# Performance work log

Hardware: AMD Instinct MI355X
Metric: run time of the kernel (lower is better)

The kernel has to match this reference:

```python
import jax, jax.numpy as jnp
import numpy as np

DIM = 128        # per-head dim == model width in this module
Q_HEADS = 16
KV_HEADS = 4
WINDOW = 512
BATCH = 4
SEQ = 2048


def setup_inputs() -> dict:
    key = jax.random.key(0)
    k1, k2, k3 = jax.random.split(key, 3)
    x = jax.random.normal(k1, (BATCH, SEQ, DIM), dtype=jnp.float32)
    # fused qkv weight, stored (in, out) so forward is x @ W_qkv
    W_qkv = jax.random.normal(k2, (DIM, (Q_HEADS + 2 * KV_HEADS) * DIM), dtype=jnp.float32) * (DIM ** -0.5)
    W_proj = jax.random.normal(k3, (Q_HEADS * DIM, DIM), dtype=jnp.float32) * ((Q_HEADS * DIM) ** -0.5)
    return {"x": x, "W_qkv": W_qkv, "W_proj": W_proj}


def _gqa_forward(x, W_qkv, W_proj):
    b, s, d = x.shape
    qkv = x @ W_qkv                                    # [b, s, (Hq+2Hkv)*d]
    qkv = qkv.reshape(b, s, Q_HEADS + 2 * KV_HEADS, d).transpose(0, 2, 1, 3)
    q = qkv[:, :Q_HEADS]                               # [b, Hq, s, d]
    k = qkv[:, Q_HEADS:Q_HEADS + KV_HEADS]             # [b, Hkv, s, d]
    v = qkv[:, Q_HEADS + KV_HEADS:]                    # [b, Hkv, s, d]

    # GQA: repeat kv heads to match q heads
    group = Q_HEADS // KV_HEADS
    k = jnp.repeat(k, group, axis=1)                   # [b, Hq, s, d]
    v = jnp.repeat(v, group, axis=1)

    scale = 1.0 / jnp.sqrt(jnp.float32(d))
    scores = jnp.einsum('bhqd,bhkd->bhqk', q, k) * scale   # [b, Hq, s, s]

    q_idx = jnp.arange(s)[:, None]
    kv_idx = jnp.arange(s)[None, :]
    rel = (q_idx - kv_idx).astype(jnp.float32)         # [s, s]
    # per-head ALiBi slope: exp2(-(h+1)*8/Hq), added (sign matches source)
    h = jnp.arange(Q_HEADS, dtype=jnp.float32)
    slopes = jnp.exp2(-((h + 1.0) * 8.0 / Q_HEADS))    # [Hq]
    scores = scores + slopes[None, :, None, None] * rel[None, None, :, :]

    mask = (q_idx >= kv_idx) & ((q_idx - kv_idx) <= WINDOW)
    scores = jnp.where(mask[None, None], scores, -jnp.inf)
    probs = jax.nn.softmax(scores, axis=-1)

    att = jnp.einsum('bhqk,bhkd->bhqd', probs, v)      # [b, Hq, s, d]
    att = att.transpose(0, 2, 1, 3).reshape(b, s, Q_HEADS * d)
    return att @ W_proj                                # [b, s, d]


def reference(x, W_qkv, W_proj):
    return _gqa_forward(x, W_qkv, W_proj)
```

## Files before the change

### kernel.cpp

```cpp
#include <hip/hip_runtime.h>
#include <math.h>

#define DIM_    128
#define QH_     16
#define KVH_    4
#define WIN_    512
#define BATCH_  4
#define SEQ_    2048
#define QKV_LD  3072

#define QB_LD   3136
#define VG_LD   2112
#define AH_LD   2112
#define WP_LD   2112

#define NX   (BATCH_*SEQ_*DIM_)
#define NWQ  (DIM_*QKV_LD)

typedef __attribute__((ext_vector_type(8))) short short8;
typedef __attribute__((ext_vector_type(4))) float f32x4;
typedef unsigned short u16;
typedef unsigned int u32;

__device__ __forceinline__ u16 f2bf(float f) {
    u32 u = __float_as_uint(f);
    u += 0x7fff + ((u >> 16) & 1);
    return (u16)(u >> 16);
}
__device__ __forceinline__ float bf2f(u16 u) {
    return __uint_as_float(((u32)u) << 16);
}
__device__ __forceinline__ u32 pkbf(float a, float b) {
    u32 r;
    __asm__("v_cvt_pk_bf16_f32 %0, %1, %2" : "=v"(r) : "v"(a), "v"(b));
    return r;
}
#define MFMA16 __builtin_amdgcn_mfma_f32_16x16x32_bf16

#if __has_builtin(__builtin_amdgcn_exp2f)
#define EXP2F __builtin_amdgcn_exp2f
#else
#define EXP2F exp2f
#endif

__device__ __forceinline__ void gload_lds16(const u16* g, u16* l) {
    __builtin_amdgcn_global_load_lds(
        (const __attribute__((address_space(1))) unsigned int*)(const void*)g,
        (__attribute__((address_space(3))) unsigned int*)(void*)l, 16, 0, 0);
}

__global__ __launch_bounds__(256) void prep(
    const float* __restrict__ x, const float* __restrict__ Wqkv,
    const float* __restrict__ Wproj,
    u16* __restrict__ xh, u16* __restrict__ wth, u16* __restrict__ wpth)
{
    if (blockIdx.x < 1024) {
        const size_t t = (size_t)blockIdx.x * 256 + threadIdx.x;
        float4 v = *(const float4*)(x + 4 * t);
        ushort4 o;
        o.x = f2bf(v.x); o.y = f2bf(v.y); o.z = f2bf(v.z); o.w = f2bf(v.w);
        *(ushort4*)(xh + 4 * t) = o;
        return;
    }
    __shared__ float T[32][33];
    int tile = blockIdx.x - 1024;
    const float* src; u16* dst; int N, ldo;
    if (tile < 384) { src = Wqkv;  dst = wth;  N = 3072; ldo = 128; }
    else { tile -= 384; src = Wproj; dst = wpth; N = 128; ldo = WP_LD; }
    const int ntile = N >> 5;
    const int k0 = (tile / ntile) << 5, n0 = (tile % ntile) << 5;
    const int tx = threadIdx.x & 31, ty = threadIdx.x >> 5;
    #pragma unroll
    for (int i = 0; i < 4; ++i)
        T[ty + 8 * i][tx] = src[(size_t)(k0 + ty + 8 * i) * N + n0 + tx];
    __syncthreads();
    #pragma unroll
    for (int i = 0; i < 4; ++i)
        dst[(size_t)(n0 + ty + 8 * i) * ldo + k0 + tx] = f2bf(T[tx][ty + 8 * i]);
}

__global__ __launch_bounds__(256) void gemm1_mfma(
    const u16* __restrict__ xh, const u16* __restrict__ wth,
    u16* __restrict__ qkvb, u16* __restrict__ vg)
{
    const int bn = blockIdx.x * 256;
    const int mc = blockIdx.y * 128;
    const int tid = threadIdx.x;
    const int wv = tid >> 6, lane = tid & 63;
    const int lo = lane & 15, hi = lane >> 4;
    const int lr = lo, quad = hi;
    const int wn = bn + wv * 64;

    __shared__ u16 Ct[2][16][264];

    short8 bf[4][4];
    #pragma unroll
    for (int nt = 0; nt < 4; ++nt)
        #pragma unroll
        for (int s = 0; s < 4; ++s)
            bf[nt][s] = *(const short8*)(
                wth + (size_t)(wn + nt * 16 + lo) * DIM_ + s * 32 + hi * 8);

    const bool qk = (bn < 2560);
    const u16* aA = xh + (size_t)(mc + lo) * DIM_ + hi * 8;
    const int sr = tid >> 4, sc = tid & 15;

#define G1BODY(AF, IT) do {                                                   \
    f32x4 acc[4] = {};                                                        \
    if (qk) {                                                                 \
        _Pragma("unroll")                                                     \
        for (int s = 0; s < 4; ++s)                                           \
            _Pragma("unroll")                                                 \
            for (int nt = 0; nt < 4; ++nt)                                    \
                acc[nt] = MFMA16(bf[nt][s], AF[s], acc[nt], 0, 0, 0);         \
        const int bufq = (IT) & 1;                                            \
        _Pragma("unroll")                                                     \
        for (int nt = 0; nt < 4; ++nt) {                                      \
            uint2 o;                                                          \
            o.x = pkbf(acc[nt][0], acc[nt][1]);                               \
            o.y = pkbf(acc[nt][2], acc[nt][3]);                               \
            *(uint2*)&Ct[bufq][lr][wv * 64 + nt * 16 + quad * 4] = o;         \
        }                                                                     \
        __syncthreads();                                                      \
        const int row = mc + (IT) * 16 + sr;                                  \
        u16* drow = qkvb + (size_t)row * QB_LD + bn;                          \
        short8 v0 = *(const short8*)&Ct[bufq][sr][sc * 8];                    \
        short8 v1 = *(const short8*)&Ct[bufq][sr][128 + sc * 8];              \
        *(short8*)(drow + sc * 8) = v0;                                       \
        *(short8*)(drow + 128 + sc * 8) = v1;                                 \
    } else {                                                                  \
        _Pragma("unroll")                                                     \
        for (int s = 0; s < 4; ++s)                                           \
            _Pragma("unroll")                                                 \
            for (int nt = 0; nt < 4; ++nt)                                    \
                acc[nt] = MFMA16(AF[s], bf[nt][s], acc[nt], 0, 0, 0);         \
        const int m0 = mc + (IT) * 16 + quad * 4;                             \
        const int bb = m0 >> 11, mseq = m0 & 2047;                            \
        _Pragma("unroll")                                                     \
        for (int nt = 0; nt < 4; ++nt) {                                      \
            const int ncol = wn + nt * 16 + lr - 2560;                        \
            const int kvh = ncol >> 7, d = ncol & 127;                        \
            uint2 o;                                                          \
            o.x = pkbf(acc[nt][0], acc[nt][1]);                               \
            o.y = pkbf(acc[nt][2], acc[nt][3]);                               \
            *(uint2*)(vg + ((size_t)(bb * KVH_ + kvh) * DIM_ + d) * VG_LD     \
                      + mseq) = o;                                            \
        }                                                                     \
    }                                                                         \
} while (0)

    short8 afA[4], afB[4];
    #pragma unroll
    for (int s = 0; s < 4; ++s) afA[s] = *(const short8*)(aA + s * 32);

    #pragma unroll 1
    for (int it = 0; it < 8; it += 2) {
        const u16* aN = aA + (size_t)(it + 1) * 16 * DIM_;
        #pragma unroll
        for (int s = 0; s < 4; ++s) afB[s] = *(const short8*)(aN + s * 32);
        G1BODY(afA, it);
        const int nx = (it + 2 < 8) ? (it + 2) : 7;
        const u16* aN2 = aA + (size_t)nx * 16 * DIM_;
        #pragma unroll
        for (int s = 0; s < 4; ++s) afA[s] = *(const short8*)(aN2 + s * 32);
        G1BODY(afB, it + 1);
    }
#undef G1BODY
}

__global__ __launch_bounds__(512) void attn_mfma(
    const u16* __restrict__ qkvb, const u16* __restrict__ vg,
    u16* __restrict__ ah)
{
    const int xcd  = blockIdx.x & 7;
    const int idx  = blockIdx.x >> 3;
    const int pair = xcd + 8 * (idx & 1);
    const int qt   = idx >> 1;
    const int b    = pair >> 2, kvh = pair & 3;
    const int q0 = qt << 5;
    const int tid = threadIdx.x;
    const int wv8 = tid >> 6, lane = tid & 63;
    const int hq = wv8 >> 1, mrow = wv8 & 1;
    const int lr = lane & 15, quad = lane >> 4;
    const int h = kvh * 4 + hq;
    const bool oddq = (quad & 1) != 0;

    __shared__ u16 Kb[3][8][512];
    __shared__ u16 Vb[3][8][512];

    const float scale2 = 0.08838834764831845f * 1.4426950408889634f;
    const float slope2 = exp2f(-0.5f * (float)(h + 1)) * 1.4426950408889634f;
    const int jbase = max(0, q0 - WIN_);
    const int nch = (q0 + 32 - jbase) >> 5;
    const size_t rowb = (size_t)b * SEQ_;
    const u16* kg  = qkvb + rowb * QB_LD + (QH_ + kvh) * DIM_;
    const u16* vgb = vg + (size_t)(b * KVH_ + kvh) * DIM_ * VG_LD;
    const int lo = lane & 15, hi = lane >> 4;

    short8 qf[4];
    {
        const u16* qp = qkvb + (rowb + q0 + mrow * 16 + lr) * QB_LD
                        + h * DIM_ + quad * 8;
        #pragma unroll
        for (int s = 0; s < 4; ++s) qf[s] = *(const short8*)(qp + 32 * s);
    }

    float alpha0;
    {
        const int q = q0 + mrow * 16 + lr;
        const int rm = (q < WIN_) ? q : WIN_;
        alpha0 = slope2 * (float)(q - rm);
    }

    f32x4 O[8] = {};
    float rs = 0.f;

    #define STAGE(CH, SLOT) do {                                              \
        const int _jk = jbase + ((CH) << 5);                                  \
        gload_lds16(kg + (size_t)(_jk + (wv8 >> 2) * 16 + lo) * QB_LD         \
                    + (wv8 & 3) * 32 + hi * 8, &Kb[(SLOT)][wv8][0]);          \
        gload_lds16(vgb + (size_t)(wv8 * 16 + lo) * VG_LD + _jk + hi * 8,     \
                    &Vb[(SLOT)][wv8][0]);                                     \
    } while (0)

    STAGE(0, 0);
    STAGE(1, 1);

    for (int ch = 0; ch < nch; ++ch) {
        const int jk = jbase + (ch << 5);
        const int slot = ch % 3;
        __asm__ volatile("s_waitcnt vmcnt(2)" ::: "memory");
        __asm__ volatile("s_barrier" ::: "memory");
        { const int cn = (ch + 2 < nch) ? (ch + 2) : (nch - 1);
          STAGE(cn, (ch + 2) % 3); }

        u32 pw[2][2];
        const int qm0 = q0 + mrow * 16;
        #pragma unroll
        for (int nt = 0; nt < 2; ++nt) {
            f32x4 c = {0.f, 0.f, 0.f, 0.f};
            __builtin_amdgcn_s_setprio(1);
            #pragma unroll
            for (int s = 0; s < 4; ++s) {
                short8 kf = *(const short8*)&Kb[slot][nt * 4 + s][lane * 8];
                c = MFMA16(kf, qf[s], c, 0, 0, 0);
            }
            __builtin_amdgcn_s_setprio(0);
            const int jknt = jk + nt * 16;
            const float b0 = fmaf(-slope2, (float)(jknt + quad * 4), alpha0);
            float e0, e1, e2, e3;
            if (qm0 >= jknt + 15 && qm0 + 15 <= jknt + WIN_) {
                e0 = EXP2F(fmaf(c[0], scale2, b0));
                e1 = EXP2F(fmaf(c[1], scale2, b0 - slope2));
                e2 = EXP2F(fmaf(c[2], scale2, b0 - 2.f * slope2));
                e3 = EXP2F(fmaf(c[3], scale2, b0 - 3.f * slope2));
            } else {
                const int q = qm0 + lr, j0q = jknt + quad * 4;
                float ee[4];
                #pragma unroll
                for (int r = 0; r < 4; ++r) {
                    const int rel = q - (j0q + r);
                    const float t = fmaf(c[r], scale2, b0 - (float)r * slope2);
                    ee[r] = ((unsigned)rel <= (unsigned)WIN_) ? EXP2F(t) : 0.f;
                }
                e0 = ee[0]; e1 = ee[1]; e2 = ee[2]; e3 = ee[3];
            }
            rs += (e0 + e1) + (e2 + e3);
            pw[nt][0] = pkbf(e0, e1);
            pw[nt][1] = pkbf(e2, e3);
        }

        short8 pa;
        {
            union { u32 w[4]; short8 s; } P;
            #pragma unroll
            for (int w = 0; w < 2; ++w) {
                auto r = __builtin_amdgcn_permlane32_swap(
                    pw[0][w], pw[1][w], false, false);
                const u32 rx = r[0], ry = r[1];
                const u32 sx = (u32)__shfl_xor((int)rx, 16);
                const u32 sy = (u32)__shfl_xor((int)ry, 16);
                P.w[w]     = oddq ? sy : rx;
                P.w[2 + w] = oddq ? ry : sx;
            }
            pa = P.s;
        }

        __builtin_amdgcn_s_setprio(1);
        #pragma unroll
        for (int nt = 0; nt < 8; ++nt) {
            short8 vf = *(const short8*)&Vb[slot][nt][lane * 8];
            O[nt] = MFMA16(vf, pa, O[nt], 0, 0, 0);
        }
        __builtin_amdgcn_s_setprio(0);
    }
    #undef STAGE

    __asm__ volatile("s_waitcnt vmcnt(0)" ::: "memory");

    rs += __shfl_xor(rs, 16);
    rs += __shfl_xor(rs, 32);

    {
        const float inv = 1.0f / rs;
        u16* dst = ah + (rowb + q0 + mrow * 16 + lr) * (size_t)AH_LD
                   + h * DIM_;
        #pragma unroll
        for (int nt = 0; nt < 8; ++nt) {
            uint2 o;
            o.x = pkbf(O[nt][0] * inv, O[nt][1] * inv);
            o.y = pkbf(O[nt][2] * inv, O[nt][3] * inv);
            *(uint2*)(dst + nt * 16 + quad * 4) = o;
        }
    }
}

__global__ __launch_bounds__(512) void gemm2_mfma(
    const u16* __restrict__ ah, const u16* __restrict__ wpth,
    float* __restrict__ out)
{
    const int bm = blockIdx.x * 32;
    const int tid = threadIdx.x;
    const int wv8 = tid >> 6, lane = tid & 63;
    const int wr = wv8 >> 2, wc = wv8 & 3;
    const int lr = lane & 15, quad = lane >> 4;

    __shared__ u16 At2[2][32][520];

    #define G2STAGE(KS, SLOT) do {                                            \
        _Pragma("unroll")                                                     \
        for (int _t = 0; _t < 4; ++_t) {                                      \
            const int _r = wv8 * 4 + _t;                                      \
            gload_lds16(ah + (size_t)(bm + _r) * AH_LD + (KS) * 512           \
                        + lane * 8, &At2[(SLOT)][_r][0]);                     \
        }                                                                     \
    } while (0)

    f32x4 acc[2] = {};

    G2STAGE(0, 0);

    #pragma unroll 1
    for (int ks = 0; ks < 4; ++ks) {
        const int slot = ks & 1;
        __asm__ volatile("s_waitcnt vmcnt(0)" ::: "memory");
        __asm__ volatile("s_barrier" ::: "memory");
        if (ks < 3) G2STAGE(ks + 1, slot ^ 1);

        const u16* wbase = wpth + (size_t)(wc * 32 + lr) * WP_LD
                           + ks * 512 + quad * 8;
        #pragma unroll
        for (int s = 0; s < 16; ++s) {
            short8 wf0 = *(const short8*)(wbase + s * 32);
            short8 wf1 = *(const short8*)(wbase + (size_t)16 * WP_LD + s * 32);
            short8 af  = *(const short8*)
                &At2[slot][wr * 16 + lr][s * 32 + quad * 8];
            acc[0] = MFMA16(wf0, af, acc[0], 0, 0, 0);
            acc[1] = MFMA16(wf1, af, acc[1], 0, 0, 0);
        }
    }
    #undef G2STAGE

    __asm__ volatile("s_waitcnt vmcnt(0)" ::: "memory");

    #pragma unroll
    for (int nt = 0; nt < 2; ++nt) {
        float* orow = out + (size_t)(bm + wr * 16 + lr) * DIM_
                      + wc * 32 + nt * 16 + quad * 4;
        *(float4*)orow = *(float4*)&acc[nt];
    }
}

extern "C" void kernel_launch(void* const* d_in, const int* in_sizes, int n_in,
                              void* d_out, int out_size, void* d_ws, size_t ws_size,
                              hipStream_t stream)
{
    const float* x     = (const float*)d_in[0];
    const float* Wqkv  = (const float*)d_in[1];
    const float* Wproj = (const float*)d_in[2];
    float* out = (float*)d_out;

    u16* xh   = (u16*)d_ws;
    u16* wth  = xh   + (size_t)NX;
    u16* wpth = wth  + (size_t)NWQ;
    u16* qkvb = wpth + (size_t)DIM_ * WP_LD;
    u16* vg   = qkvb + (size_t)8192 * QB_LD;
    u16* ahp  = vg   + (size_t)BATCH_ * KVH_ * DIM_ * VG_LD;

    prep<<<1024 + 640, 256, 0, stream>>>(x, Wqkv, Wproj, xh, wth, wpth);

    gemm1_mfma<<<dim3(12, 64), 256, 0, stream>>>(xh, wth, qkvb, vg);

    attn_mfma<<<1024, 512, 0, stream>>>(qkvb, vg, ahp);

    gemm2_mfma<<<8192 / 32, 512, 0, stream>>>(ahp, wpth, out);
}
```

Measured before the change: 184.8 us.

## Widen attention KV chunks to 64 keys with double-buffered LDS staging

Each loop iteration of the attention kernel now handles 64 keys instead of 32, and the shared-memory pipeline moves from three 32-key slots to two 64-key slots. Each chunk is loaded fully, with a wait on all outstanding loads before the barrier, and the next chunk is prefetched. This halves the number of barriers and loop iterations and gives each wave more MFMA work between syncs. The cost is reduced prefetch depth, since only one chunk is in flight and vmcnt(0) exposes more load latency. Rows and columns past the sequence end are clamped, and the masking handles the extra keys, which adds some wasted compute at the window edges.

```diff
diff --git a/kernel.cpp b/kernel.cpp
--- a/kernel.cpp
+++ b/kernel.cpp
@@ -185,15 +185,15 @@
     const int h = kvh * 4 + hq;
     const bool oddq = (quad & 1) != 0;
 
-    __shared__ u16 Kb[3][8][512];
-    __shared__ u16 Vb[3][8][512];
+    __shared__ u16 Kb[2][16][512];
+    __shared__ u16 Vb[2][16][512];
 
     const float scale2 = 0.08838834764831845f * 1.4426950408889634f;
     const float slope2 = exp2f(-0.5f * (float)(h + 1)) * 1.4426950408889634f;
     const int jbase = max(0, q0 - WIN_);
-    const int nch = (q0 + 32 - jbase) >> 5;
+    const int nch = (q0 + 32 - jbase + 63) >> 6;
     const size_t rowb = (size_t)b * SEQ_;
-    const u16* kg  = qkvb + rowb * QB_LD + (QH_ + kvh) * DIM_;
+    const u16* kgp = qkvb + rowb * QB_LD + (QH_ + kvh) * DIM_;
     const u16* vgb = vg + (size_t)(b * KVH_ + kvh) * DIM_ * VG_LD;
     const int lo = lane & 15, hi = lane >> 4;
 
@@ -216,28 +216,34 @@
     float rs = 0.f;
 
     #define STAGE(CH, SLOT) do {                                              \
-        const int _jk = jbase + ((CH) << 5);                                  \
-        gload_lds16(kg + (size_t)(_jk + (wv8 >> 2) * 16 + lo) * QB_LD         \
-                    + (wv8 & 3) * 32 + hi * 8, &Kb[(SLOT)][wv8][0]);          \
-        gload_lds16(vgb + (size_t)(wv8 * 16 + lo) * VG_LD + _jk + hi * 8,     \
-                    &Vb[(SLOT)][wv8][0]);                                     \
+        const int _jk = jbase + ((CH) << 6);                                  \
+        _Pragma("unroll")                                                     \
+        for (int _t = 0; _t < 2; ++_t) {                                      \
+            const int _p = wv8 + _t * 8;                                      \
+            int _kr = _jk + (_p >> 2) * 16 + lo;                              \
+            _kr = (_kr < SEQ_) ? _kr : (SEQ_ - 1);                            \
+            gload_lds16(kgp + (size_t)_kr * QB_LD + (_p & 3) * 32 + hi * 8,   \
+                        &Kb[(SLOT)][_p][0]);                                  \
+            int _kc = _jk + (_p & 1) * 32 + hi * 8;                           \
+            _kc = (_kc < SEQ_ - 8) ? _kc : (SEQ_ - 8);                        \
+            gload_lds16(vgb + (size_t)((_p >> 1) * 16 + lo) * VG_LD + _kc,    \
+                        &Vb[(SLOT)][_p][0]);                                  \
+        }                                                                     \
     } while (0)
 
     STAGE(0, 0);
-    STAGE(1, 1);
 
     for (int ch = 0; ch < nch; ++ch) {
-        const int jk = jbase + (ch << 5);
-        const int slot = ch % 3;
-        __asm__ volatile("s_waitcnt vmcnt(2)" ::: "memory");
+        const int jk = jbase + (ch << 6);
+        const int slot = ch & 1;
+        __asm__ volatile("s_waitcnt vmcnt(0)" ::: "memory");
         __asm__ volatile("s_barrier" ::: "memory");
-        { const int cn = (ch + 2 < nch) ? (ch + 2) : (nch - 1);
-          STAGE(cn, (ch + 2) % 3); }
-
-        u32 pw[2][2];
+        if (ch + 1 < nch) STAGE(ch + 1, slot ^ 1);
+
+        u32 pw[4][2];
         const int qm0 = q0 + mrow * 16;
         #pragma unroll
-        for (int nt = 0; nt < 2; ++nt) {
+        for (int nt = 0; nt < 4; ++nt) {
             f32x4 c = {0.f, 0.f, 0.f, 0.f};
             __builtin_amdgcn_s_setprio(1);
             #pragma unroll
@@ -270,27 +276,30 @@
             pw[nt][1] = pkbf(e2, e3);
         }
 
-        short8 pa;
-        {
+        short8 pa[2];
+        #pragma unroll
+        for (int g = 0; g < 2; ++g) {
             union { u32 w[4]; short8 s; } P;
             #pragma unroll
             for (int w = 0; w < 2; ++w) {
                 auto r = __builtin_amdgcn_permlane32_swap(
-                    pw[0][w], pw[1][w], false, false);
+                    pw[2 * g][w], pw[2 * g + 1][w], false, false);
                 const u32 rx = r[0], ry = r[1];
                 const u32 sx = (u32)__shfl_xor((int)rx, 16);
                 const u32 sy = (u32)__shfl_xor((int)ry, 16);
                 P.w[w]     = oddq ? sy : rx;
                 P.w[2 + w] = oddq ? ry : sx;
             }
-            pa = P.s;
+            pa[g] = P.s;
         }
 
         __builtin_amdgcn_s_setprio(1);
         #pragma unroll
         for (int nt = 0; nt < 8; ++nt) {
-            short8 vf = *(const short8*)&Vb[slot][nt][lane * 8];
-            O[nt] = MFMA16(vf, pa, O[nt], 0, 0, 0);
+            short8 vf0 = *(const short8*)&Vb[slot][nt * 2][lane * 8];
+            short8 vf1 = *(const short8*)&Vb[slot][nt * 2 + 1][lane * 8];
+            O[nt] = MFMA16(vf0, pa[0], O[nt], 0, 0, 0);
+            O[nt] = MFMA16(vf1, pa[1], O[nt], 0, 0, 0);
         }
         __builtin_amdgcn_s_setprio(0);
     }
```

Measured after the change: 179.3 us. 3.0% less time.
